# Kernel tuning notes

Measured on AMD Instinct MI355X. Metric: run time of the kernel, lower is better.

## Reference

```python
import jax, jax.numpy as jnp
import numpy as np

B, S, H = 512, 200, 256

def setup_inputs() -> dict:
    key = jax.random.key(0)
    ks = jax.random.split(key, 7)
    scale = 1.0 / np.sqrt(H)
    return {
        "all_memory": jax.random.normal(ks[0], (B, S, H), dtype=jnp.float32),
        "last_memory": jax.random.normal(ks[1], (B, H), dtype=jnp.float32),
        "U": jax.random.normal(ks[2], (H, H), dtype=jnp.float32) * scale,   # U_meta weight
        "W": jax.random.normal(ks[3], (H, H), dtype=jnp.float32) * scale,   # W_meta weight
        "V": jax.random.normal(ks[4], (H, 1), dtype=jnp.float32) * scale,   # V_meta weight (stored as [H,1])
        "MetaW": jax.random.normal(ks[5], (4, H), dtype=jnp.float32) * scale,  # Meta weight
        "Metab": jax.random.normal(ks[6], (4,), dtype=jnp.float32) * scale,    # Meta bias ('multiple' mode)
    }

def reference(all_memory, last_memory, U, W, V, MetaW, Metab):
    # U_meta(all_memory): [B,S,H]; W_meta(last_memory): [B,H] broadcast over S
    a = jnp.einsum('bsh,kh->bsk', all_memory, U)
    l = jnp.einsum('bh,kh->bk', last_memory, W)
    # additive attention score: V_meta(tanh(a + l)) -> [B,S]
    scores = jnp.einsum('bsh,h->bs', jnp.tanh(a + l[:, None, :]), V[:, 0])
    alpha = jax.nn.softmax(scores, axis=1)  # softmax over seq dim
    pooled = jnp.einsum('bs,bsh->bh', alpha, all_memory)  # weighted sum of values
    return pooled @ MetaW.T + Metab  # [B, 4]
```

## Files before the change

kernel.cpp:

```cpp
#include <hip/hip_runtime.h>
#include <hip/hip_bf16.h>
#include <math.h>

#define NB 512
#define NS 200
#define NH 256
#define TILE_S 32
#define NTILE 7
#define LDSPAD 8
#define LDW (NH + LDSPAD)

#define OFF_SC 0
#define OFF_L  (NB * NS)
#define OFF_UB (OFF_L + NB * NH)
#define WS_FLOATS_PRE (OFF_UB + (NH * NH) / 2)
#define WS_FLOATS_MIN (NB * NS)

typedef __bf16 bf16x8 __attribute__((ext_vector_type(8)));
typedef float  f32x4  __attribute__((ext_vector_type(4)));

__device__ __forceinline__ float tanh_fast(float x) {
  float xc = fminf(fmaxf(x, -10.f), 10.f);
  float e  = __expf(2.f * xc);
  return (e - 1.f) / (e + 1.f);
}

__global__ __launch_bounds__(256)
void precompute(const float* __restrict__ lastm, const float* __restrict__ W,
                const float* __restrict__ U,
                float* __restrict__ l_ws, __bf16* __restrict__ Uswz)
{
  const int t = threadIdx.x;
  if (blockIdx.x < NB) {
    const int b = blockIdx.x;
    __shared__ float lm_sm[NH];
    lm_sm[t] = lastm[(size_t)b * NH + t];
    __syncthreads();
    const float4* wrow = (const float4*)(W + (size_t)t * NH);
    const float4* lrow = (const float4*)lm_sm;
    float a0 = 0.f, a1 = 0.f, a2 = 0.f, a3 = 0.f;
#pragma unroll 8
    for (int i = 0; i < NH / 4; ++i) {
      float4 w4 = wrow[i];
      float4 m4 = lrow[i];
      a0 = fmaf(w4.x, m4.x, a0);
      a1 = fmaf(w4.y, m4.y, a1);
      a2 = fmaf(w4.z, m4.z, a2);
      a3 = fmaf(w4.w, m4.w, a3);
    }
    l_ws[(size_t)b * NH + t] = (a0 + a1) + (a2 + a3);
  } else {
    const int id    = (blockIdx.x - NB) * 256 + t;
    const int n_blk = id >> 9;
    const int kk    = (id >> 6) & 7;
    const int lane  = id & 63;
    const int row   = n_blk * 16 + (lane & 15);
    const int col   = kk * 32 + (lane >> 4) * 8;
    const float4* s = (const float4*)(U + (size_t)row * NH + col);
    const float4 a = s[0], c = s[1];
    bf16x8 pk;
    pk[0] = (__bf16)a.x; pk[1] = (__bf16)a.y;
    pk[2] = (__bf16)a.z; pk[3] = (__bf16)a.w;
    pk[4] = (__bf16)c.x; pk[5] = (__bf16)c.y;
    pk[6] = (__bf16)c.z; pk[7] = (__bf16)c.w;
    *(bf16x8*)(Uswz + (size_t)id * 8) = pk;
  }
}

template<bool PRE>
__global__ __launch_bounds__(256, 2)
void scores_kernel(const float* __restrict__ mem,
                   const float* __restrict__ lastm,
                   const float* __restrict__ U,
                   const float* __restrict__ W,
                   const float* __restrict__ V,
                   const float* __restrict__ l_ws,
                   const __bf16* __restrict__ Uswz,
                   float* __restrict__ scores)
{
  const int blk  = blockIdx.x;
  const int b    = blk / NTILE;
  const int tile = blk - b * NTILE;
  const int s0   = tile * TILE_S;
  const int rows = min(TILE_S, NS - s0);

  const int t    = threadIdx.x;
  const int wave = t >> 6;
  const int lane = t & 63;
  const int m16  = lane & 15;
  const int quad = lane >> 4;

  __shared__ __align__(16) __bf16 mem_sm[TILE_S][LDW];
  __shared__ float swave_sm[4][TILE_S];
  __shared__ float l_sm[NH];
  __shared__ float lm_sm[NH];

  if (!PRE) {
    lm_sm[t] = lastm[(size_t)b * NH + t];
    __syncthreads();
    const float4* wrow = (const float4*)(W + (size_t)t * NH);
    const float4* lrow = (const float4*)lm_sm;
    float a0 = 0.f, a1 = 0.f, a2 = 0.f, a3 = 0.f;
#pragma unroll 8
    for (int i = 0; i < NH / 4; ++i) {
      float4 w4 = wrow[i];
      float4 m4 = lrow[i];
      a0 = fmaf(w4.x, m4.x, a0);
      a1 = fmaf(w4.y, m4.y, a1);
      a2 = fmaf(w4.z, m4.z, a2);
      a3 = fmaf(w4.w, m4.w, a3);
    }
    l_sm[t] = (a0 + a1) + (a2 + a3);
    __syncthreads();
  }

  float l_reg[4], v_reg[4];
#pragma unroll
  for (int nf = 0; nf < 4; ++nf) {
    const int n = wave * 64 + nf * 16 + m16;
    l_reg[nf] = PRE ? l_ws[(size_t)b * NH + n] : l_sm[n];
    v_reg[nf] = V[n];
  }

  bf16x8 u_frag[4][8];
  if (PRE) {
    const __bf16* uw = Uswz + ((size_t)(wave * 4 * 8 * 64) + lane) * 8;
#pragma unroll
    for (int nf = 0; nf < 4; ++nf)
#pragma unroll
      for (int kk = 0; kk < 8; ++kk)
        u_frag[nf][kk] = *(const bf16x8*)(uw + (size_t)((nf * 8 + kk) << 9));
  } else {
#pragma unroll
    for (int nf = 0; nf < 4; ++nf) {
      const int n = wave * 64 + nf * 16 + m16;
      const float* urow = U + (size_t)n * NH;
#pragma unroll
      for (int kk = 0; kk < 8; ++kk) {
        const float4 lo = *(const float4*)(urow + kk * 32 + quad * 8);
        const float4 hi = *(const float4*)(urow + kk * 32 + quad * 8 + 4);
        bf16x8 f;
        f[0] = (__bf16)lo.x; f[1] = (__bf16)lo.y;
        f[2] = (__bf16)lo.z; f[3] = (__bf16)lo.w;
        f[4] = (__bf16)hi.x; f[5] = (__bf16)hi.y;
        f[6] = (__bf16)hi.z; f[7] = (__bf16)hi.w;
        u_frag[nf][kk] = f;
      }
    }
  }

  const float4* src4 = (const float4*)(mem + ((size_t)b * NS + s0) * NH);
#pragma unroll
  for (int i = 0; i < 4; ++i) {
    const int f2  = i * 256 + t;
    const int row = f2 >> 5;
    const int c8  = (f2 & 31) * 8;
    bf16x8 pk;
    if (row < rows) {
      const float4 a = src4[f2 * 2];
      const float4 c = src4[f2 * 2 + 1];
      pk[0] = (__bf16)a.x; pk[1] = (__bf16)a.y;
      pk[2] = (__bf16)a.z; pk[3] = (__bf16)a.w;
      pk[4] = (__bf16)c.x; pk[5] = (__bf16)c.y;
      pk[6] = (__bf16)c.z; pk[7] = (__bf16)c.w;
    } else {
      pk = (bf16x8)(__bf16)0.f;
    }
    *(bf16x8*)&mem_sm[row][c8] = pk;
  }
  __syncthreads();

  f32x4 acc[2][4];
  const f32x4 fzero = {0.f, 0.f, 0.f, 0.f};
#pragma unroll
  for (int mt = 0; mt < 2; ++mt)
#pragma unroll
    for (int nf = 0; nf < 4; ++nf)
      acc[mt][nf] = fzero;

#pragma unroll
  for (int kk = 0; kk < 8; ++kk) {
    const int c = kk * 32 + quad * 8;
    bf16x8 a0 = *(const bf16x8*)&mem_sm[m16][c];
    bf16x8 a1 = *(const bf16x8*)&mem_sm[16 + m16][c];
#pragma unroll
    for (int nf = 0; nf < 4; ++nf) {
      acc[0][nf] = __builtin_amdgcn_mfma_f32_16x16x32_bf16(a0, u_frag[nf][kk], acc[0][nf], 0, 0, 0);
      acc[1][nf] = __builtin_amdgcn_mfma_f32_16x16x32_bf16(a1, u_frag[nf][kk], acc[1][nf], 0, 0, 0);
    }
  }

  float p[2][4];
#pragma unroll
  for (int mt = 0; mt < 2; ++mt) {
#pragma unroll
    for (int reg = 0; reg < 4; ++reg) {
      float s = 0.f;
#pragma unroll
      for (int nf = 0; nf < 4; ++nf)
        s = fmaf(tanh_fast(acc[mt][nf][reg] + l_reg[nf]), v_reg[nf], s);
      p[mt][reg] = s;
    }
  }
#pragma unroll
  for (int off = 1; off < 16; off <<= 1) {
#pragma unroll
    for (int mt = 0; mt < 2; ++mt)
#pragma unroll
      for (int reg = 0; reg < 4; ++reg)
        p[mt][reg] += __shfl_xor(p[mt][reg], off);
  }
  if (m16 == 0) {
#pragma unroll
    for (int mt = 0; mt < 2; ++mt)
#pragma unroll
      for (int reg = 0; reg < 4; ++reg)
        swave_sm[wave][mt * 16 + quad * 4 + reg] = p[mt][reg];
  }
  __syncthreads();

  if (t < rows)
    scores[(size_t)b * NS + s0 + t] =
        swave_sm[0][t] + swave_sm[1][t] + swave_sm[2][t] + swave_sm[3][t];
}

__global__ __launch_bounds__(512)
void softmax_pool(const float* __restrict__ scores,
                  const float* __restrict__ mem,
                  const float* __restrict__ MetaW,
                  const float* __restrict__ Metab,
                  float* __restrict__ out)
{
  const int b    = blockIdx.x;
  const int t    = threadIdx.x;
  const int wave = t >> 6;
  const int lane = t & 63;

  __shared__ float alpha_sm[NS];
  __shared__ float red_sm[8];
  __shared__ __align__(16) float part_sm[8][NH];
  __shared__ float pooled_sm[NH];

  float sv = (t < NS) ? scores[(size_t)b * NS + t] : -INFINITY;

  float wm = sv;
#pragma unroll
  for (int off = 32; off > 0; off >>= 1)
    wm = fmaxf(wm, __shfl_xor(wm, off));
  if (lane == 0) red_sm[wave] = wm;
  __syncthreads();
  float m = red_sm[0];
#pragma unroll
  for (int w = 1; w < 8; ++w) m = fmaxf(m, red_sm[w]);

  float e = (t < NS) ? __expf(sv - m) : 0.f;
  float wsum = e;
#pragma unroll
  for (int off = 32; off > 0; off >>= 1)
    wsum += __shfl_xor(wsum, off);
  __syncthreads();
  if (lane == 0) red_sm[wave] = wsum;
  __syncthreads();
  float Z = 0.f;
#pragma unroll
  for (int w = 0; w < 8; ++w) Z += red_sm[w];
  const float Zi = 1.f / Z;

  if (t < NS) alpha_sm[t] = e * Zi;
  __syncthreads();

  f32x4 acc4 = {0.f, 0.f, 0.f, 0.f};
  const f32x4* memb = (const f32x4*)(mem + (size_t)b * NS * NH);
  for (int r = wave; r < NS; r += 8) {
    const float a = alpha_sm[r];
    const f32x4 v4 = memb[(size_t)r * (NH / 4) + lane];
    acc4[0] = fmaf(a, v4[0], acc4[0]);
    acc4[1] = fmaf(a, v4[1], acc4[1]);
    acc4[2] = fmaf(a, v4[2], acc4[2]);
    acc4[3] = fmaf(a, v4[3], acc4[3]);
  }
  *(f32x4*)&part_sm[wave][lane * 4] = acc4;
  __syncthreads();

  if (t < NH) {
    float s = 0.f;
#pragma unroll
    for (int w = 0; w < 8; ++w) s += part_sm[w][t];
    pooled_sm[t] = s;
  }
  __syncthreads();

  if (wave < 4) {
    float s = 0.f;
#pragma unroll
    for (int i = 0; i < 4; ++i) {
      const int h = i * 64 + lane;
      s = fmaf(pooled_sm[h], MetaW[(size_t)wave * NH + h], s);
    }
#pragma unroll
    for (int off = 32; off > 0; off >>= 1)
      s += __shfl_down(s, off);
    if (lane == 0)
      out[b * 4 + wave] = s + Metab[wave];
  }
}

extern "C" void kernel_launch(void* const* d_in, const int* in_sizes, int n_in,
                              void* d_out, int out_size, void* d_ws, size_t ws_size,
                              hipStream_t stream) {
  const float* mem   = (const float*)d_in[0];
  const float* lastm = (const float*)d_in[1];
  const float* U     = (const float*)d_in[2];
  const float* W     = (const float*)d_in[3];
  const float* V     = (const float*)d_in[4];
  const float* MetaW = (const float*)d_in[5];
  const float* Metab = (const float*)d_in[6];
  float* out = (float*)d_out;
  float* ws  = (float*)d_ws;

  float* scores = ws + OFF_SC;

  if (ws_size >= (size_t)WS_FLOATS_PRE * sizeof(float)) {
    float*  l_ws = ws + OFF_L;
    __bf16* Uswz = (__bf16*)(ws + OFF_UB);
    hipLaunchKernelGGL(precompute, dim3(NB + 32), dim3(256), 0, stream,
                       lastm, W, U, l_ws, Uswz);
    hipLaunchKernelGGL(scores_kernel<true>, dim3(NB * NTILE), dim3(256), 0, stream,
                       mem, lastm, U, W, V, l_ws, Uswz, scores);
  } else {
    hipLaunchKernelGGL(scores_kernel<false>, dim3(NB * NTILE), dim3(256), 0, stream,
                       mem, lastm, U, W, V, (const float*)nullptr, (const __bf16*)nullptr, scores);
  }
  hipLaunchKernelGGL(softmax_pool, dim3(NB), dim3(512), 0, stream,
                     scores, mem, MetaW, Metab, out);
}
```

Baseline: 213.9 us.

## Split scores kernel over hidden-dim chunks with partial score reduction in softmax

Each scores block now covers 64 sequence rows and one quarter of the 256 hidden outputs, instead of 32 rows and all outputs. Per-wave U fragments drop from 32 to 8 registers, which should ease register pressure and raise occupancy. Each block writes a partial score per chunk, and softmax_pool sums the four partials with one float4 load. The cost is that every memory tile is loaded and converted to bf16 four times, once per chunk block. Work on zero-padded rows also grows, since the last 64-row tile holds only 8 valid rows.

```diff
diff --git a/kernel.cpp b/kernel.cpp
--- a/kernel.cpp
+++ b/kernel.cpp
@@ -5,16 +5,16 @@
 #define NB 512
 #define NS 200
 #define NH 256
-#define TILE_S 32
-#define NTILE 7
+#define TILE_S 64
+#define NSTILE 4
+#define NCHUNK 4
 #define LDSPAD 8
 #define LDW (NH + LDSPAD)
 
-#define OFF_SC 0
-#define OFF_L  (NB * NS)
-#define OFF_UB (OFF_L + NB * NH)
+#define OFF_PART 0
+#define OFF_L    (NB * NS * NCHUNK)
+#define OFF_UB   (OFF_L + NB * NH)
 #define WS_FLOATS_PRE (OFF_UB + (NH * NH) / 2)
-#define WS_FLOATS_MIN (NB * NS)
 
 typedef __bf16 bf16x8 __attribute__((ext_vector_type(8)));
 typedef float  f32x4  __attribute__((ext_vector_type(4)));
@@ -76,13 +76,14 @@
                    const float* __restrict__ V,
                    const float* __restrict__ l_ws,
                    const __bf16* __restrict__ Uswz,
-                   float* __restrict__ scores)
+                   float* __restrict__ part)
 {
-  const int blk  = blockIdx.x;
-  const int b    = blk / NTILE;
-  const int tile = blk - b * NTILE;
-  const int s0   = tile * TILE_S;
-  const int rows = min(TILE_S, NS - s0);
+  const int blk   = blockIdx.x;
+  const int chunk = blk & 3;
+  const int stile = (blk >> 2) & 3;
+  const int b     = blk >> 4;
+  const int s0    = stile * TILE_S;
+  const int rows  = min(TILE_S, NS - s0);
 
   const int t    = threadIdx.x;
   const int wave = t >> 6;
@@ -90,16 +91,16 @@
   const int m16  = lane & 15;
   const int quad = lane >> 4;
 
+  const int n_blk = chunk * 4 + wave;
+  const int n     = n_blk * 16 + m16;
+
   __shared__ __align__(16) __bf16 mem_sm[TILE_S][LDW];
   __shared__ float swave_sm[4][TILE_S];
   __shared__ float l_sm[NH];
-  __shared__ float lm_sm[NH];
 
   if (!PRE) {
-    lm_sm[t] = lastm[(size_t)b * NH + t];
-    __syncthreads();
     const float4* wrow = (const float4*)(W + (size_t)t * NH);
-    const float4* lrow = (const float4*)lm_sm;
+    const float4* lrow = (const float4*)(lastm + (size_t)b * NH);
     float a0 = 0.f, a1 = 0.f, a2 = 0.f, a3 = 0.f;
 #pragma unroll 8
     for (int i = 0; i < NH / 4; ++i) {
@@ -114,44 +115,33 @@
     __syncthreads();
   }
 
-  float l_reg[4], v_reg[4];
-#pragma unroll
-  for (int nf = 0; nf < 4; ++nf) {
-    const int n = wave * 64 + nf * 16 + m16;
-    l_reg[nf] = PRE ? l_ws[(size_t)b * NH + n] : l_sm[n];
-    v_reg[nf] = V[n];
-  }
-
-  bf16x8 u_frag[4][8];
+  const float l_reg = PRE ? l_ws[(size_t)b * NH + n] : l_sm[n];
+  const float v_reg = V[n];
+
+  bf16x8 u_frag[8];
   if (PRE) {
-    const __bf16* uw = Uswz + ((size_t)(wave * 4 * 8 * 64) + lane) * 8;
-#pragma unroll
-    for (int nf = 0; nf < 4; ++nf)
-#pragma unroll
-      for (int kk = 0; kk < 8; ++kk)
-        u_frag[nf][kk] = *(const bf16x8*)(uw + (size_t)((nf * 8 + kk) << 9));
+    const __bf16* uw = Uswz + ((size_t)(n_blk * 8 * 64) + lane) * 8;
+#pragma unroll
+    for (int kk = 0; kk < 8; ++kk)
+      u_frag[kk] = *(const bf16x8*)(uw + (size_t)(kk << 9));
   } else {
-#pragma unroll
-    for (int nf = 0; nf < 4; ++nf) {
-      const int n = wave * 64 + nf * 16 + m16;
-      const float* urow = U + (size_t)n * NH;
-#pragma unroll
-      for (int kk = 0; kk < 8; ++kk) {
-        const float4 lo = *(const float4*)(urow + kk * 32 + quad * 8);
-        const float4 hi = *(const float4*)(urow + kk * 32 + quad * 8 + 4);
-        bf16x8 f;
-        f[0] = (__bf16)lo.x; f[1] = (__bf16)lo.y;
-        f[2] = (__bf16)lo.z; f[3] = (__bf16)lo.w;
-        f[4] = (__bf16)hi.x; f[5] = (__bf16)hi.y;
-        f[6] = (__bf16)hi.z; f[7] = (__bf16)hi.w;
-        u_frag[nf][kk] = f;
-      }
+    const float* urow = U + (size_t)n * NH;
+#pragma unroll
+    for (int kk = 0; kk < 8; ++kk) {
+      const float4 lo = *(const float4*)(urow + kk * 32 + quad * 8);
+      const float4 hi = *(const float4*)(urow + kk * 32 + quad * 8 + 4);
+      bf16x8 f;
+      f[0] = (__bf16)lo.x; f[1] = (__bf16)lo.y;
+      f[2] = (__bf16)lo.z; f[3] = (__bf16)lo.w;
+      f[4] = (__bf16)hi.x; f[5] = (__bf16)hi.y;
+      f[6] = (__bf16)hi.z; f[7] = (__bf16)hi.w;
+      u_frag[kk] = f;
     }
   }
 
   const float4* src4 = (const float4*)(mem + ((size_t)b * NS + s0) * NH);
 #pragma unroll
-  for (int i = 0; i < 4; ++i) {
+  for (int i = 0; i < 8; ++i) {
     const int f2  = i * 256 + t;
     const int row = f2 >> 5;
     const int c8  = (f2 & 31) * 8;
@@ -170,62 +160,55 @@
   }
   __syncthreads();
 
-  f32x4 acc[2][4];
+  f32x4 acc[4];
   const f32x4 fzero = {0.f, 0.f, 0.f, 0.f};
 #pragma unroll
-  for (int mt = 0; mt < 2; ++mt)
-#pragma unroll
-    for (int nf = 0; nf < 4; ++nf)
-      acc[mt][nf] = fzero;
+  for (int mt = 0; mt < 4; ++mt) acc[mt] = fzero;
 
 #pragma unroll
   for (int kk = 0; kk < 8; ++kk) {
     const int c = kk * 32 + quad * 8;
     bf16x8 a0 = *(const bf16x8*)&mem_sm[m16][c];
     bf16x8 a1 = *(const bf16x8*)&mem_sm[16 + m16][c];
-#pragma unroll
-    for (int nf = 0; nf < 4; ++nf) {
-      acc[0][nf] = __builtin_amdgcn_mfma_f32_16x16x32_bf16(a0, u_frag[nf][kk], acc[0][nf], 0, 0, 0);
-      acc[1][nf] = __builtin_amdgcn_mfma_f32_16x16x32_bf16(a1, u_frag[nf][kk], acc[1][nf], 0, 0, 0);
-    }
-  }
-
-  float p[2][4];
-#pragma unroll
-  for (int mt = 0; mt < 2; ++mt) {
-#pragma unroll
-    for (int reg = 0; reg < 4; ++reg) {
-      float s = 0.f;
-#pragma unroll
-      for (int nf = 0; nf < 4; ++nf)
-        s = fmaf(tanh_fast(acc[mt][nf][reg] + l_reg[nf]), v_reg[nf], s);
-      p[mt][reg] = s;
-    }
-  }
+    bf16x8 a2 = *(const bf16x8*)&mem_sm[32 + m16][c];
+    bf16x8 a3 = *(const bf16x8*)&mem_sm[48 + m16][c];
+    acc[0] = __builtin_amdgcn_mfma_f32_16x16x32_bf16(a0, u_frag[kk], acc[0], 0, 0, 0);
+    acc[1] = __builtin_amdgcn_mfma_f32_16x16x32_bf16(a1, u_frag[kk], acc[1], 0, 0, 0);
+    acc[2] = __builtin_amdgcn_mfma_f32_16x16x32_bf16(a2, u_frag[kk], acc[2], 0, 0, 0);
+    acc[3] = __builtin_amdgcn_mfma_f32_16x16x32_bf16(a3, u_frag[kk], acc[3], 0, 0, 0);
+  }
+
+  float p[4][4];
+#pragma unroll
+  for (int mt = 0; mt < 4; ++mt)
+#pragma unroll
+    for (int reg = 0; reg < 4; ++reg)
+      p[mt][reg] = tanh_fast(acc[mt][reg] + l_reg) * v_reg;
+
 #pragma unroll
   for (int off = 1; off < 16; off <<= 1) {
 #pragma unroll
-    for (int mt = 0; mt < 2; ++mt)
+    for (int mt = 0; mt < 4; ++mt)
 #pragma unroll
       for (int reg = 0; reg < 4; ++reg)
         p[mt][reg] += __shfl_xor(p[mt][reg], off);
   }
   if (m16 == 0) {
 #pragma unroll
-    for (int mt = 0; mt < 2; ++mt)
+    for (int mt = 0; mt < 4; ++mt)
 #pragma unroll
       for (int reg = 0; reg < 4; ++reg)
         swave_sm[wave][mt * 16 + quad * 4 + reg] = p[mt][reg];
   }
   __syncthreads();
 
-  if (t < rows)
-    scores[(size_t)b * NS + s0 + t] =
+  if (t < TILE_S && t < rows)
+    part[((size_t)b * NS + s0 + t) * NCHUNK + chunk] =
         swave_sm[0][t] + swave_sm[1][t] + swave_sm[2][t] + swave_sm[3][t];
 }
 
 __global__ __launch_bounds__(512)
-void softmax_pool(const float* __restrict__ scores,
+void softmax_pool(const float* __restrict__ part,
                   const float* __restrict__ mem,
                   const float* __restrict__ MetaW,
                   const float* __restrict__ Metab,
@@ -241,7 +224,11 @@
   __shared__ __align__(16) float part_sm[8][NH];
   __shared__ float pooled_sm[NH];
 
-  float sv = (t < NS) ? scores[(size_t)b * NS + t] : -INFINITY;
+  float sv = -INFINITY;
+  if (t < NS) {
+    const float4 p4 = *(const float4*)(part + ((size_t)b * NS + t) * NCHUNK);
+    sv = (p4.x + p4.y) + (p4.z + p4.w);
+  }
 
   float wm = sv;
 #pragma unroll
@@ -318,19 +305,19 @@
   float* out = (float*)d_out;
   float* ws  = (float*)d_ws;
 
-  float* scores = ws + OFF_SC;
+  float* part = ws + OFF_PART;
 
   if (ws_size >= (size_t)WS_FLOATS_PRE * sizeof(float)) {
     float*  l_ws = ws + OFF_L;
     __bf16* Uswz = (__bf16*)(ws + OFF_UB);
     hipLaunchKernelGGL(precompute, dim3(NB + 32), dim3(256), 0, stream,
                        lastm, W, U, l_ws, Uswz);
-    hipLaunchKernelGGL(scores_kernel<true>, dim3(NB * NTILE), dim3(256), 0, stream,
-                       mem, lastm, U, W, V, l_ws, Uswz, scores);
+    hipLaunchKernelGGL(scores_kernel<true>, dim3(NB * NSTILE * NCHUNK), dim3(256), 0, stream,
+                       mem, lastm, U, W, V, l_ws, Uswz, part);
   } else {
-    hipLaunchKernelGGL(scores_kernel<false>, dim3(NB * NTILE), dim3(256), 0, stream,
-                       mem, lastm, U, W, V, (const float*)nullptr, (const __bf16*)nullptr, scores);
+    hipLaunchKernelGGL(scores_kernel<false>, dim3(NB * NSTILE * NCHUNK), dim3(256), 0, stream,
+                       mem, lastm, U, W, V, (const float*)nullptr, (const __bf16*)nullptr, part);
   }
   hipLaunchKernelGGL(softmax_pool, dim3(NB), dim3(512), 0, stream,
-                     scores, mem, MetaW, Metab, out);
-}
+                     part, mem, MetaW, Metab, out);
+}
```

Measured after the change: 248.5 us. 1.16x slower.

## Chunk U fragments over N loop to cut register pressure

Applied to the files above, without the earlier changes.

Instead of holding all 32 bf16x8 U fragments (4 N-blocks x 8 K-steps) in registers per wave, the kernel now loops over 4 N-chunks and loads 8 fragments per chunk, running the MFMA and tanh/V reduction per chunk. This cuts VGPR usage and should raise occupancy. In exchange the U loads are serialized with compute inside the loop, and the N-block assignment to waves is interleaved. It also drops the LDS staging of last_memory in the non-precompute path and reads it directly from global memory.

```diff
diff --git a/kernel.cpp b/kernel.cpp
--- a/kernel.cpp
+++ b/kernel.cpp
@@ -7,6 +7,7 @@
 #define NH 256
 #define TILE_S 32
 #define NTILE 7
+#define NCHUNK 4
 #define LDSPAD 8
 #define LDW (NH + LDSPAD)
 
@@ -14,7 +15,6 @@
 #define OFF_L  (NB * NS)
 #define OFF_UB (OFF_L + NB * NH)
 #define WS_FLOATS_PRE (OFF_UB + (NH * NH) / 2)
-#define WS_FLOATS_MIN (NB * NS)
 
 typedef __bf16 bf16x8 __attribute__((ext_vector_type(8)));
 typedef float  f32x4  __attribute__((ext_vector_type(4)));
@@ -93,13 +93,10 @@
   __shared__ __align__(16) __bf16 mem_sm[TILE_S][LDW];
   __shared__ float swave_sm[4][TILE_S];
   __shared__ float l_sm[NH];
-  __shared__ float lm_sm[NH];
 
   if (!PRE) {
-    lm_sm[t] = lastm[(size_t)b * NH + t];
-    __syncthreads();
     const float4* wrow = (const float4*)(W + (size_t)t * NH);
-    const float4* lrow = (const float4*)lm_sm;
+    const float4* lrow = (const float4*)(lastm + (size_t)b * NH);
     float a0 = 0.f, a1 = 0.f, a2 = 0.f, a3 = 0.f;
 #pragma unroll 8
     for (int i = 0; i < NH / 4; ++i) {
@@ -112,41 +109,6 @@
     }
     l_sm[t] = (a0 + a1) + (a2 + a3);
     __syncthreads();
-  }
-
-  float l_reg[4], v_reg[4];
-#pragma unroll
-  for (int nf = 0; nf < 4; ++nf) {
-    const int n = wave * 64 + nf * 16 + m16;
-    l_reg[nf] = PRE ? l_ws[(size_t)b * NH + n] : l_sm[n];
-    v_reg[nf] = V[n];
-  }
-
-  bf16x8 u_frag[4][8];
-  if (PRE) {
-    const __bf16* uw = Uswz + ((size_t)(wave * 4 * 8 * 64) + lane) * 8;
-#pragma unroll
-    for (int nf = 0; nf < 4; ++nf)
-#pragma unroll
-      for (int kk = 0; kk < 8; ++kk)
-        u_frag[nf][kk] = *(const bf16x8*)(uw + (size_t)((nf * 8 + kk) << 9));
-  } else {
-#pragma unroll
-    for (int nf = 0; nf < 4; ++nf) {
-      const int n = wave * 64 + nf * 16 + m16;
-      const float* urow = U + (size_t)n * NH;
-#pragma unroll
-      for (int kk = 0; kk < 8; ++kk) {
-        const float4 lo = *(const float4*)(urow + kk * 32 + quad * 8);
-        const float4 hi = *(const float4*)(urow + kk * 32 + quad * 8 + 4);
-        bf16x8 f;
-        f[0] = (__bf16)lo.x; f[1] = (__bf16)lo.y;
-        f[2] = (__bf16)lo.z; f[3] = (__bf16)lo.w;
-        f[4] = (__bf16)hi.x; f[5] = (__bf16)hi.y;
-        f[6] = (__bf16)hi.z; f[7] = (__bf16)hi.w;
-        u_frag[nf][kk] = f;
-      }
-    }
   }
 
   const float4* src4 = (const float4*)(mem + ((size_t)b * NS + s0) * NH);
@@ -170,38 +132,60 @@
   }
   __syncthreads();
 
-  f32x4 acc[2][4];
-  const f32x4 fzero = {0.f, 0.f, 0.f, 0.f};
+  float p[2][4];
 #pragma unroll
   for (int mt = 0; mt < 2; ++mt)
 #pragma unroll
-    for (int nf = 0; nf < 4; ++nf)
-      acc[mt][nf] = fzero;
-
-#pragma unroll
-  for (int kk = 0; kk < 8; ++kk) {
-    const int c = kk * 32 + quad * 8;
-    bf16x8 a0 = *(const bf16x8*)&mem_sm[m16][c];
-    bf16x8 a1 = *(const bf16x8*)&mem_sm[16 + m16][c];
-#pragma unroll
-    for (int nf = 0; nf < 4; ++nf) {
-      acc[0][nf] = __builtin_amdgcn_mfma_f32_16x16x32_bf16(a0, u_frag[nf][kk], acc[0][nf], 0, 0, 0);
-      acc[1][nf] = __builtin_amdgcn_mfma_f32_16x16x32_bf16(a1, u_frag[nf][kk], acc[1][nf], 0, 0, 0);
-    }
-  }
-
-  float p[2][4];
-#pragma unroll
-  for (int mt = 0; mt < 2; ++mt) {
-#pragma unroll
-    for (int reg = 0; reg < 4; ++reg) {
-      float s = 0.f;
-#pragma unroll
-      for (int nf = 0; nf < 4; ++nf)
-        s = fmaf(tanh_fast(acc[mt][nf][reg] + l_reg[nf]), v_reg[nf], s);
-      p[mt][reg] = s;
-    }
-  }
+    for (int reg = 0; reg < 4; ++reg)
+      p[mt][reg] = 0.f;
+
+  for (int chunk = 0; chunk < NCHUNK; ++chunk) {
+    const int n_blk = chunk * 4 + wave;
+    const int n     = n_blk * 16 + m16;
+
+    bf16x8 u_frag[8];
+    if (PRE) {
+      const __bf16* uw = Uswz + ((size_t)(n_blk * 8 * 64) + lane) * 8;
+#pragma unroll
+      for (int kk = 0; kk < 8; ++kk)
+        u_frag[kk] = *(const bf16x8*)(uw + (size_t)(kk << 9));
+    } else {
+      const float* urow = U + (size_t)n * NH;
+#pragma unroll
+      for (int kk = 0; kk < 8; ++kk) {
+        const float4 lo = *(const float4*)(urow + kk * 32 + quad * 8);
+        const float4 hi = *(const float4*)(urow + kk * 32 + quad * 8 + 4);
+        bf16x8 f;
+        f[0] = (__bf16)lo.x; f[1] = (__bf16)lo.y;
+        f[2] = (__bf16)lo.z; f[3] = (__bf16)lo.w;
+        f[4] = (__bf16)hi.x; f[5] = (__bf16)hi.y;
+        f[6] = (__bf16)hi.z; f[7] = (__bf16)hi.w;
+        u_frag[kk] = f;
+      }
+    }
+
+    const float l_reg = PRE ? l_ws[(size_t)b * NH + n] : l_sm[n];
+    const float v_reg = V[n];
+
+    f32x4 acc[2];
+    const f32x4 fzero = {0.f, 0.f, 0.f, 0.f};
+    acc[0] = fzero; acc[1] = fzero;
+#pragma unroll
+    for (int kk = 0; kk < 8; ++kk) {
+      const int c = kk * 32 + quad * 8;
+      bf16x8 a0 = *(const bf16x8*)&mem_sm[m16][c];
+      bf16x8 a1 = *(const bf16x8*)&mem_sm[16 + m16][c];
+      acc[0] = __builtin_amdgcn_mfma_f32_16x16x32_bf16(a0, u_frag[kk], acc[0], 0, 0, 0);
+      acc[1] = __builtin_amdgcn_mfma_f32_16x16x32_bf16(a1, u_frag[kk], acc[1], 0, 0, 0);
+    }
+
+#pragma unroll
+    for (int mt = 0; mt < 2; ++mt)
+#pragma unroll
+      for (int reg = 0; reg < 4; ++reg)
+        p[mt][reg] = fmaf(tanh_fast(acc[mt][reg] + l_reg), v_reg, p[mt][reg]);
+  }
+
 #pragma unroll
   for (int off = 1; off < 16; off <<= 1) {
 #pragma unroll
```

New measurement: 215.6 us. No clear change (+0.8%).
